# Kernel tuning notes

Measured on AMD Instinct MI355X. Metric: run time of the kernel, lower is better.

## Reference

```python
import jax, jax.numpy as jnp
import numpy as np

N = 4096; D0 = 1024; D1 = 1280; H0 = 819; H1 = 1024; S = 819; K = 5


def setup_inputs() -> dict:
    key = jax.random.key(0)
    ks = jax.random.split(key, 20)
    def rn(k, shape, scale=1.0):
        return jax.random.normal(k, shape, dtype=jnp.float32) * scale
    inp = {}
    inp['x0'] = rn(ks[0], (N, D0))
    inp['x1'] = rn(ks[1], (N, D1))
    inp['we'] = jax.random.uniform(ks[2], (N, 2), dtype=jnp.float32, minval=0.1, maxval=1.0)
    # scale graphs ~1/100 so row-aggregated features stay in tanh's linear-ish range
    inp['g0'] = rn(ks[3], (N, N), 0.01)
    inp['g1'] = rn(ks[4], (N, N), 0.01)
    # Linear weights stored [in, out] (torch Linear applies x @ W.T + b); xavier-ish scale
    inp['We1_0'] = rn(ks[5], (D0, H0), D0 ** -0.5); inp['be1_0'] = jnp.zeros((H0,), jnp.float32)
    inp['We2_0'] = rn(ks[6], (H0, S), H0 ** -0.5);  inp['be2_0'] = jnp.zeros((S,), jnp.float32)
    inp['We1_1'] = rn(ks[7], (D1, H1), D1 ** -0.5); inp['be1_1'] = jnp.zeros((H1,), jnp.float32)
    inp['We2_1'] = rn(ks[8], (H1, S), H1 ** -0.5);  inp['be2_1'] = jnp.zeros((S,), jnp.float32)
    inp['Wd1_0'] = rn(ks[9], (S, H0), S ** -0.5);   inp['bd1_0'] = jnp.zeros((H0,), jnp.float32)
    inp['Wd2_0'] = rn(ks[10], (H0, D0), H0 ** -0.5); inp['bd2_0'] = jnp.zeros((D0,), jnp.float32)
    inp['Wd1_1'] = rn(ks[11], (S, H1), S ** -0.5);  inp['bd1_1'] = jnp.zeros((H1,), jnp.float32)
    inp['Wd2_1'] = rn(ks[12], (H1, D1), H1 ** -0.5); inp['bd2_1'] = jnp.zeros((D1,), jnp.float32)
    inp['Ww_0'] = rn(ks[13], (S, S), S ** -0.5)
    inp['Ww_1'] = rn(ks[14], (S, S), S ** -0.5)
    inp['Wf_0'] = rn(ks[15], (S, S), S ** -0.5)
    inp['Wf_1'] = rn(ks[16], (S, S), S ** -0.5)
    # stands in for the sklearn spectral-clustering centers (constant w.r.t. autodiff)
    inp['cluster_layer'] = rn(ks[17], (K, S), 0.1)
    return inp


def _gconv2(g, x, W1, b1, W2, b2):
    # tanh(Linear(g @ x)) twice: fusable gather-MLP chain
    h1 = jnp.tanh((g @ x) @ W1 + b1)
    return jnp.tanh((g @ h1) @ W2 + b2)


def reference(x0, x1, we, g0, g1,
              We1_0, be1_0, We2_0, be2_0, We1_1, be1_1, We2_1, be2_1,
              Wd1_0, bd1_0, Wd2_0, bd2_0, Wd1_1, bd1_1, Wd2_1, bd2_1,
              Ww_0, Ww_1, Wf_0, Wf_1, cluster_layer):
    # encoders
    h2_0 = _gconv2(g0, x0, We1_0, be1_0, We2_0, be2_0)  # [N, S]
    h2_1 = _gconv2(g1, x1, We1_1, be1_1, We2_1, be2_1)  # [N, S]
    # diag(we[:,i]) @ h_i  ==  broadcast row-scale (avoids O(N^2) diag matmul)
    weighted_sum = we[:, 0:1] * h2_0 + we[:, 1:2] * h2_1
    z = weighted_sum / jnp.sum(we, axis=1, keepdims=True)  # diag(1/sum) @ ws
    # inner-product adjacency decoders
    adj0 = jax.nn.sigmoid((z @ Ww_0) @ z.T)  # [N, N]
    adj1 = jax.nn.sigmoid((z @ Ww_1) @ z.T)
    # feature decoders with fusion weights
    rec0 = _gconv2(g0, jnp.tanh(z @ Wf_0), Wd1_0, bd1_0, Wd2_0, bd2_0)  # [N, D0]
    rec1 = _gconv2(g1, jnp.tanh(z @ Wf_1), Wd1_1, bd1_1, Wd2_1, bd2_1)  # [N, D1]
    # Student-t soft assignment to cluster centers
    d2 = jnp.sum((z[:, None, :] - cluster_layer[None, :, :]) ** 2, axis=2)  # [N, K]
    q = 1.0 / (1.0 + d2)
    q = q / jnp.sum(q, axis=1, keepdims=True)
    # target distribution p
    w = q ** 2 / jnp.sum(q, axis=0)
    p = w / jnp.sum(w, axis=1, keepdims=True)
    return (rec0, rec1, adj0, adj1, z, p, q, cluster_layer)
```

## Files before the change

### kernel.cpp

```cpp
#include <hip/hip_runtime.h>
#include <hip/hip_bf16.h>
#include <cstdint>
#include <cstddef>

typedef __bf16 bf16;
typedef __attribute__((ext_vector_type(8))) __bf16 bf16x8;
typedef __attribute__((ext_vector_type(4))) __bf16 bf16x4;
typedef __attribute__((ext_vector_type(4))) float f32x4;

__device__ __forceinline__ void gload_lds16(const void* g, void* l) {
  __builtin_amdgcn_global_load_lds(
      (const __attribute__((address_space(1))) uint32_t*)(uintptr_t)g,
      (__attribute__((address_space(3))) uint32_t*)(uintptr_t)l, 16, 0, 0);
}

__device__ __forceinline__ float actf(float v, int act) {
  if (act == 1) return tanhf(v);
  if (act == 2) return 1.f / (1.f + __expf(-v));
  return v;
}

struct GProb {
  const bf16* A; const bf16* Bt; const float* bias;
  float* Cf; bf16* Cb; float* Cp;
  int K, Npad, ldcf, ldcb, Ntrue, act;
};
struct GBatch { GProb p[4]; };

template<int SPLIT>
__global__ __launch_bounds__(256, 2)
void gemm_nt_batch(GBatch b)
{
  const int nx = gridDim.x, ny = gridDim.y, nzz = gridDim.z;
  const int total = nx * ny * nzz;
  const int fid = (int)blockIdx.x + nx * ((int)blockIdx.y + ny * (int)blockIdx.z);
  const int q = total >> 3, r = total & 7;
  const int xcd = fid & 7, idx = fid >> 3;
  const int wid = (xcd < r ? xcd * (q + 1) : r * (q + 1) + (xcd - r) * q) + idx;
  const int wx = wid % nx;
  const int rest = wid / nx;
  const int wy = rest % ny;
  const int wz = rest / ny;

  const int prob = (SPLIT == 2) ? (wz >> 1) : wz;
  const int kz   = (SPLIT == 2) ? (wz & 1) : 0;
  const GProb P = b.p[prob];
  const long bn = (long)wx * 128;
  if (bn >= P.Npad) return;

  __shared__ __align__(16) bf16 As[128 * 64];
  __shared__ __align__(16) bf16 Bs[128 * 64];

  const int K    = P.K;
  const int tid  = threadIdx.x;
  const int lane = tid & 63, wave = tid >> 6;
  const int wr = wave >> 1, wc = wave & 1;
  const int l15 = lane & 15, quad = lane >> 4;
  const long bm = (long)wy * 128;

  long aoff[4], boff[4];
  int ldsoff[4];
#pragma unroll
  for (int s = 0; s < 4; ++s) {
    int slot = s * 256 + tid;
    int row = slot >> 3, cs = slot & 7;
    int gc = cs ^ (row & 7);
    aoff[s] = (bm + row) * (long)K + gc * 8;
    boff[s] = (bn + row) * (long)K + gc * 8;
    ldsoff[s] = (s * 256 + wave * 64) * 8;
  }

  const int cfr0 = ((0 * 4 + quad) ^ (l15 & 7)) * 8;
  const int cfr1 = ((1 * 4 + quad) ^ (l15 & 7)) * 8;
  int afr[2][4], bfr[2][4];
#pragma unroll
  for (int i = 0; i < 4; ++i) {
    afr[0][i] = (wr * 64 + i * 16 + l15) * 64 + cfr0;
    afr[1][i] = (wr * 64 + i * 16 + l15) * 64 + cfr1;
    bfr[0][i] = (wc * 64 + i * 16 + l15) * 64 + cfr0;
    bfr[1][i] = (wc * 64 + i * 16 + l15) * 64 + cfr1;
  }

  f32x4 acc[4][4];
#pragma unroll
  for (int i = 0; i < 4; ++i)
#pragma unroll
    for (int j = 0; j < 4; ++j) acc[i][j] = {0.f, 0.f, 0.f, 0.f};

  const int Kseg = K / SPLIT;
  const int kbeg = kz * Kseg;
  for (int k0 = kbeg; k0 < kbeg + Kseg; k0 += 64) {
    __syncthreads();
#pragma unroll
    for (int s = 0; s < 4; ++s) {
      gload_lds16(P.A + aoff[s] + k0, As + ldsoff[s]);
      gload_lds16(P.Bt + boff[s] + k0, Bs + ldsoff[s]);
    }
    __syncthreads();

#pragma unroll
    for (int ks = 0; ks < 2; ++ks) {
      bf16x8 av[4], bv[4];
#pragma unroll
      for (int i = 0; i < 4; ++i) av[i] = *(const bf16x8*)(As + afr[ks][i]);
#pragma unroll
      for (int j = 0; j < 4; ++j) bv[j] = *(const bf16x8*)(Bs + bfr[ks][j]);
#pragma unroll
      for (int i = 0; i < 4; ++i)
#pragma unroll
        for (int j = 0; j < 4; ++j)
          acc[i][j] = __builtin_amdgcn_mfma_f32_16x16x32_bf16(av[i], bv[j], acc[i][j], 0, 0, 0);
    }
  }

  const long row0 = bm + wr * 64 + quad * 4;
  const long col0 = bn + wc * 64 + l15;
  if constexpr (SPLIT == 2) {
    float* Cp = P.Cp + (long)kz * 4096 * P.Npad;
#pragma unroll
    for (int i = 0; i < 4; ++i)
#pragma unroll
      for (int j = 0; j < 4; ++j)
#pragma unroll
        for (int t = 0; t < 4; ++t)
          Cp[(row0 + i * 16 + t) * (long)P.Npad + col0 + j * 16] = acc[i][j][t];
  } else {
    const int act = P.act;
#pragma unroll
    for (int i = 0; i < 4; ++i) {
#pragma unroll
      for (int j = 0; j < 4; ++j) {
        long c = col0 + j * 16;
        float bb = P.bias ? P.bias[c] : 0.f;
#pragma unroll
        for (int t = 0; t < 4; ++t) {
          long r = row0 + i * 16 + t;
          float v = actf(acc[i][j][t] + bb, act);
          if (P.Cf && c < P.Ntrue) P.Cf[r * P.ldcf + c] = v;
          if (P.Cb) P.Cb[r * P.ldcb + c] = (bf16)v;
        }
      }
    }
  }
}

struct CProb {
  const float* part; const float* bias;
  float* Cf; bf16* Cb;
  int Npad, ldcf, ldcb, Ntrue, act;
};
struct CBatch { CProb p[2]; };

__global__ void combine_batch(CBatch cb)
{
  const CProb P = cb.p[blockIdx.z];
  const int row = blockIdx.x;
  const int c4 = threadIdx.x * 4;
  if (c4 >= P.Npad) return;
  const long base = (long)row * P.Npad + c4;
  float4 a = *(const float4*)(P.part + base);
  float4 b = *(const float4*)(P.part + (long)4096 * P.Npad + base);
  float v[4] = {a.x + b.x, a.y + b.y, a.z + b.z, a.w + b.w};
  if (P.bias) {
    float4 bi = *(const float4*)(P.bias + c4);
    v[0] += bi.x; v[1] += bi.y; v[2] += bi.z; v[3] += bi.w;
  }
#pragma unroll
  for (int t = 0; t < 4; ++t) v[t] = actf(v[t], P.act);
  if (P.Cf && c4 < P.Ntrue) {
    float* o = P.Cf + (long)row * P.ldcf + c4;
    o[0] = v[0]; o[1] = v[1]; o[2] = v[2]; o[3] = v[3];
  }
  if (P.Cb) {
    bf16x4 o = {(bf16)v[0], (bf16)v[1], (bf16)v[2], (bf16)v[3]};
    *(bf16x4*)(P.Cb + (long)row * P.ldcb + c4) = o;
  }
}

__global__ void combz(const float* __restrict__ pA, const float* __restrict__ pB,
                      const float* __restrict__ bA, const float* __restrict__ bB,
                      const float* __restrict__ we, float* __restrict__ zout,
                      bf16* __restrict__ zb)
{
  const int n = blockIdx.x;
  const int c = threadIdx.x * 4;
  const long base = (long)n * 896 + c;
  const long half = (long)4096 * 896;
  float4 a0 = *(const float4*)(pA + base);
  float4 a1 = *(const float4*)(pA + half + base);
  float4 b0 = *(const float4*)(pB + base);
  float4 b1 = *(const float4*)(pB + half + base);
  float4 ba = *(const float4*)(bA + c);
  float4 bb = *(const float4*)(bB + c);
  const float w0 = we[n * 2], w1 = we[n * 2 + 1];
  const float inv = 1.f / (w0 + w1);
  float h0[4] = {a0.x + a1.x + ba.x, a0.y + a1.y + ba.y, a0.z + a1.z + ba.z, a0.w + a1.w + ba.w};
  float h1[4] = {b0.x + b1.x + bb.x, b0.y + b1.y + bb.y, b0.z + b1.z + bb.z, b0.w + b1.w + bb.w};
  bf16x4 o;
#pragma unroll
  for (int t = 0; t < 4; ++t) {
    float v = (w0 * tanhf(h0[t]) + w1 * tanhf(h1[t])) * inv;
    o[t] = (bf16)v;
    if (c + t < 819) zout[(long)n * 819 + c + t] = v;
  }
  *(bf16x4*)(zb + base) = o;
}

struct TrBatch {
  const void* src[14]; bf16* dst[14];
  int R[14], C[14], Q[14], nbx[14], isb[14];
  int blkStart[15];
  int nprob;
};

__global__ void tr_batch(TrBatch a)
{
  __shared__ float tile[32][33];
  int pi = 0, b = blockIdx.x;
  while (b >= a.blkStart[pi + 1]) ++pi;
  const int rel = b - a.blkStart[pi];
  const int nbx = a.nbx[pi];
  const int q0 = (rel % nbx) * 32;
  const int p0 = (rel / nbx) * 32;
  const int R = a.R[pi], C = a.C[pi], Q = a.Q[pi];
  const bool isb = a.isb[pi] != 0;
  const void* src = a.src[pi];
  const int tx = threadIdx.x & 31, ty = threadIdx.x >> 5;
#pragma unroll
  for (int y = ty; y < 32; y += 8) {
    int r = q0 + y, c = p0 + tx;
    float v = 0.f;
    if (r < R && c < C)
      v = isb ? (float)((const bf16*)src)[(long)r * C + c]
              : ((const float*)src)[(long)r * C + c];
    tile[y][tx] = v;
  }
  __syncthreads();
  bf16* dst = a.dst[pi];
#pragma unroll
  for (int y = ty; y < 32; y += 8)
    dst[(long)(p0 + y) * Q + (q0 + tx)] = (bf16)tile[tx][y];
}

struct CvtB { const float* s[4]; bf16* d[4]; long n[4]; };
__global__ void cvt_batch(CvtB cb)
{
  const float* s = cb.s[blockIdx.z];
  bf16* d = cb.d[blockIdx.z];
  long i = ((long)blockIdx.x * blockDim.x + threadIdx.x) * 4;
  if (i >= cb.n[blockIdx.z]) return;
  float4 v = *(const float4*)(s + i);
  bf16x4 o = {(bf16)v.x, (bf16)v.y, (bf16)v.z, (bf16)v.w};
  *(bf16x4*)(d + i) = o;
}

__global__ void qkern(const float* __restrict__ z, const float* __restrict__ cl,
                      float* __restrict__ qout)
{
  const int n = blockIdx.x;
  const int lane = threadIdx.x;
  float d0 = 0, d1 = 0, d2 = 0, d3 = 0, d4 = 0;
  for (int s = lane; s < 819; s += 64) {
    float zv = z[(long)n * 819 + s];
    float t0 = zv - cl[0 * 819 + s]; d0 += t0 * t0;
    float t1 = zv - cl[1 * 819 + s]; d1 += t1 * t1;
    float t2 = zv - cl[2 * 819 + s]; d2 += t2 * t2;
    float t3 = zv - cl[3 * 819 + s]; d3 += t3 * t3;
    float t4 = zv - cl[4 * 819 + s]; d4 += t4 * t4;
  }
#pragma unroll
  for (int off = 32; off > 0; off >>= 1) {
    d0 += __shfl_xor(d0, off);
    d1 += __shfl_xor(d1, off);
    d2 += __shfl_xor(d2, off);
    d3 += __shfl_xor(d3, off);
    d4 += __shfl_xor(d4, off);
  }
  if (lane == 0) {
    float q0 = 1.f / (1.f + d0), q1 = 1.f / (1.f + d1), q2 = 1.f / (1.f + d2);
    float q3 = 1.f / (1.f + d3), q4 = 1.f / (1.f + d4);
    float inv = 1.f / (q0 + q1 + q2 + q3 + q4);
    float* qr = qout + (long)n * 5;
    qr[0] = q0 * inv; qr[1] = q1 * inv; qr[2] = q2 * inv;
    qr[3] = q3 * inv; qr[4] = q4 * inv;
  }
}

__global__ void colsum_kern(const float* __restrict__ q, float* __restrict__ colsum)
{
  __shared__ float red[256];
  const int k = blockIdx.x;
  float s = 0.f;
  for (int n = threadIdx.x; n < 4096; n += 256) s += q[(long)n * 5 + k];
  red[threadIdx.x] = s;
  __syncthreads();
  for (int w = 128; w > 0; w >>= 1) {
    if (threadIdx.x < w) red[threadIdx.x] += red[threadIdx.x + w];
    __syncthreads();
  }
  if (threadIdx.x == 0) colsum[k] = red[0];
}

__global__ void pkern(const float* __restrict__ q, const float* __restrict__ colsum,
                      float* __restrict__ p)
{
  int n = blockIdx.x * blockDim.x + threadIdx.x;
  if (n >= 4096) return;
  float w[5], s = 0.f;
#pragma unroll
  for (int k = 0; k < 5; ++k) {
    float qv = q[(long)n * 5 + k];
    w[k] = qv * qv / colsum[k];
    s += w[k];
  }
  float inv = 1.f / s;
#pragma unroll
  for (int k = 0; k < 5; ++k) p[(long)n * 5 + k] = w[k] * inv;
}

struct BiasArgs {
  const float* src[8];
  float* dst[8];
  int n[8];
  int np[8];
};

__global__ void biaspad(BiasArgs a)
{
  int b = blockIdx.x;
  for (int i = threadIdx.x; i < a.np[b]; i += blockDim.x)
    a.dst[b][i] = (i < a.n[b]) ? a.src[b][i] : 0.f;
}

extern "C" void kernel_launch(void* const* d_in, const int* in_sizes, int n_in,
                              void* d_out, int out_size, void* d_ws, size_t ws_size,
                              hipStream_t stream)
{
  (void)in_sizes; (void)n_in; (void)out_size; (void)ws_size;
  const float* x0    = (const float*)d_in[0];
  const float* x1    = (const float*)d_in[1];
  const float* we    = (const float*)d_in[2];
  const float* g0    = (const float*)d_in[3];
  const float* g1    = (const float*)d_in[4];
  const float* We1_0 = (const float*)d_in[5];
  const float* be1_0 = (const float*)d_in[6];
  const float* We2_0 = (const float*)d_in[7];
  const float* be2_0 = (const float*)d_in[8];
  const float* We1_1 = (const float*)d_in[9];
  const float* be1_1 = (const float*)d_in[10];
  const float* We2_1 = (const float*)d_in[11];
  const float* be2_1 = (const float*)d_in[12];
  const float* Wd1_0 = (const float*)d_in[13];
  const float* bd1_0 = (const float*)d_in[14];
  const float* Wd2_0 = (const float*)d_in[15];
  const float* bd2_0 = (const float*)d_in[16];
  const float* Wd1_1 = (const float*)d_in[17];
  const float* bd1_1 = (const float*)d_in[18];
  const float* Wd2_1 = (const float*)d_in[19];
  const float* bd2_1 = (const float*)d_in[20];
  const float* Ww0   = (const float*)d_in[21];
  const float* Ww1   = (const float*)d_in[22];
  const float* Wf0   = (const float*)d_in[23];
  const float* Wf1   = (const float*)d_in[24];
  const float* clus  = (const float*)d_in[25];
  float* out = (float*)d_out;

  const size_t OFF_REC0 = 0;
  const size_t OFF_REC1 = 4194304;
  const size_t OFF_ADJ0 = 9437184;
  const size_t OFF_ADJ1 = 26214400;
  const size_t OFF_Z    = 42991616;
  const size_t OFF_P    = 46346240;
  const size_t OFF_Q    = 46366720;
  const size_t OFF_CL   = 46387200;

  char* ws = (char*)d_ws;
  size_t off = 0;
  auto alloc = [&](size_t bytes) -> void* {
    off = (off + 255) & ~(size_t)255;
    void* p = ws + off;
    off += bytes;
    return p;
  };
  const long N = 4096;
  bf16* g0b   = (bf16*)alloc((size_t)N * 4096 * 2);
  bf16* g1b   = (bf16*)alloc((size_t)N * 4096 * 2);
  bf16* x0b   = (bf16*)alloc((size_t)N * 1024 * 2);
  bf16* x1b   = (bf16*)alloc((size_t)N * 1280 * 2);
  bf16* BTe10 = (bf16*)alloc((size_t)896 * 1024 * 2);
  bf16* BTe20 = (bf16*)alloc((size_t)896 * 896 * 2);
  bf16* BTe11 = (bf16*)alloc((size_t)1024 * 1280 * 2);
  bf16* BTe21 = (bf16*)alloc((size_t)896 * 1024 * 2);
  bf16* BTd10 = (bf16*)alloc((size_t)896 * 896 * 2);
  bf16* BTd20 = (bf16*)alloc((size_t)1024 * 896 * 2);
  bf16* BTd11 = (bf16*)alloc((size_t)1024 * 896 * 2);
  bf16* BTd21 = (bf16*)alloc((size_t)1280 * 1024 * 2);
  bf16* BTw0  = (bf16*)alloc((size_t)896 * 896 * 2);
  bf16* BTw1  = (bf16*)alloc((size_t)896 * 896 * 2);
  bf16* BTf0  = (bf16*)alloc((size_t)896 * 896 * 2);
  bf16* BTf1  = (bf16*)alloc((size_t)896 * 896 * 2);
  float* pbe10 = (float*)alloc(896 * 4);
  float* pbe20 = (float*)alloc(896 * 4);
  float* pbe11 = (float*)alloc(1024 * 4);
  float* pbe21 = (float*)alloc(896 * 4);
  float* pbd10 = (float*)alloc(896 * 4);
  float* pbd20 = (float*)alloc(1024 * 4);
  float* pbd11 = (float*)alloc(1024 * 4);
  float* pbd21 = (float*)alloc(1280 * 4);
  bf16* zb     = (bf16*)alloc((size_t)N * 896 * 2);
  float* colsum = (float*)alloc(64);
  bf16* xT0 = (bf16*)alloc((size_t)1024 * 4096 * 2);
  bf16* xT1 = (bf16*)alloc((size_t)1280 * 4096 * 2);
  bf16* u0  = (bf16*)alloc((size_t)N * 1024 * 2);
  bf16* u1  = (bf16*)alloc((size_t)N * 1280 * 2);
  bf16* h0  = (bf16*)alloc((size_t)N * 896 * 2);
  bf16* h1b = (bf16*)alloc((size_t)N * 1024 * 2);
  bf16* y0  = (bf16*)alloc((size_t)N * 896 * 2);
  bf16* y1  = (bf16*)alloc((size_t)N * 896 * 2);
  bf16* t0b = (bf16*)alloc((size_t)N * 896 * 2);
  bf16* t1b = (bf16*)alloc((size_t)N * 896 * 2);
  float* partA = (float*)alloc((size_t)2 * N * 1024 * 4);
  float* partB = (float*)alloc((size_t)2 * N * 1024 * 4);

  {
    CvtB cb;
    cb.s[0] = g0; cb.d[0] = g0b; cb.n[0] = N * 4096;
    cb.s[1] = g1; cb.d[1] = g1b; cb.n[1] = N * 4096;
    cb.s[2] = x0; cb.d[2] = x0b; cb.n[2] = N * 1024;
    cb.s[3] = x1; cb.d[3] = x1b; cb.n[3] = N * 1280;
    cvt_batch<<<dim3(16384, 1, 4), 256, 0, stream>>>(cb);
  }

  {
    TrBatch tb{};
    tb.nprob = 0; tb.blkStart[0] = 0;
    auto addTr = [&](const void* s, bf16* d, int R, int C, int P, int Q, int isb) {
      int i = tb.nprob++;
      tb.src[i] = s; tb.dst[i] = d;
      tb.R[i] = R; tb.C[i] = C; tb.Q[i] = Q; tb.isb[i] = isb;
      tb.nbx[i] = Q / 32;
      tb.blkStart[i + 1] = tb.blkStart[i] + (Q / 32) * (P / 32);
    };
    addTr(We1_0, BTe10, 1024, 819, 896, 1024, 0);
    addTr(We2_0, BTe20, 819, 819, 896, 896, 0);
    addTr(We1_1, BTe11, 1280, 1024, 1024, 1280, 0);
    addTr(We2_1, BTe21, 1024, 819, 896, 1024, 0);
    addTr(Wd1_0, BTd10, 819, 819, 896, 896, 0);
    addTr(Wd2_0, BTd20, 819, 1024, 1024, 896, 0);
    addTr(Wd1_1, BTd11, 819, 1024, 1024, 896, 0);
    addTr(Wd2_1, BTd21, 1024, 1280, 1280, 1024, 0);
    addTr(Ww0, BTw0, 819, 819, 896, 896, 0);
    addTr(Ww1, BTw1, 819, 819, 896, 896, 0);
    addTr(Wf0, BTf0, 819, 819, 896, 896, 0);
    addTr(Wf1, BTf1, 819, 819, 896, 896, 0);
    tr_batch<<<tb.blkStart[tb.nprob], 256, 0, stream>>>(tb);
  }

  BiasArgs ba;
  {
    const float* bsrc[8] = {be1_0, be2_0, be1_1, be2_1, bd1_0, bd2_0, bd1_1, bd2_1};
    float* bdst[8] = {pbe10, pbe20, pbe11, pbe21, pbd10, pbd20, pbd11, pbd21};
    int bn_[8] = {819, 819, 1024, 819, 819, 1024, 1024, 1280};
    int bnp[8] = {896, 896, 1024, 896, 896, 1024, 1024, 1280};
    for (int i = 0; i < 8; ++i) { ba.src[i] = bsrc[i]; ba.dst[i] = bdst[i]; ba.n[i] = bn_[i]; ba.np[i] = bnp[i]; }
  }
  biaspad<<<8, 256, 0, stream>>>(ba);

  GBatch gb{};
  int np = 0, maxN = 0;
  auto beg = [&]() { np = 0; maxN = 0; gb = GBatch{}; };
  auto add = [&](const bf16* A, const bf16* Bt, const float* bias,
                 float* Cf, int ldcf, bf16* Cb, int ldcb,
                 int K, int Npad, int Ntrue, int act) {
    gb.p[np].A = A; gb.p[np].Bt = Bt; gb.p[np].bias = bias;
    gb.p[np].Cf = Cf; gb.p[np].Cb = Cb; gb.p[np].Cp = nullptr;
    gb.p[np].K = K; gb.p[np].Npad = Npad;
    gb.p[np].ldcf = ldcf; gb.p[np].ldcb = ldcb;
    gb.p[np].Ntrue = Ntrue; gb.p[np].act = act;
    ++np;
    if (Npad > maxN) maxN = Npad;
  };
  auto addS = [&](const bf16* A, const bf16* Bt, float* Cp, int K, int Npad) {
    gb.p[np].A = A; gb.p[np].Bt = Bt; gb.p[np].bias = nullptr;
    gb.p[np].Cf = nullptr; gb.p[np].Cb = nullptr; gb.p[np].Cp = Cp;
    gb.p[np].K = K; gb.p[np].Npad = Npad;
    gb.p[np].ldcf = 0; gb.p[np].ldcb = 0; gb.p[np].Ntrue = 0; gb.p[np].act = 0;
    ++np;
    if (Npad > maxN) maxN = Npad;
  };
  auto goN = [&]() { gemm_nt_batch<1><<<dim3(maxN / 128, 32, np), 256, 0, stream>>>(gb); };
  auto goS = [&]() { gemm_nt_batch<2><<<dim3(maxN / 128, 32, np * 2), 256, 0, stream>>>(gb); };
  auto comb = [&](const float* bias0, float* Cf0, int ldf0, int Nt0, bf16* Cb0, int ldb0, int Np0, int act0,
                  const float* bias1, float* Cf1, int ldf1, int Nt1, bf16* Cb1, int ldb1, int Np1, int act1) {
    CBatch cb;
    cb.p[0] = {partA, bias0, Cf0, Cb0, Np0, ldf0, ldb0, Nt0, act0};
    cb.p[1] = {partB, bias1, Cf1, Cb1, Np1, ldf1, ldb1, Nt1, act1};
    combine_batch<<<dim3(4096, 1, 2), 256, 0, stream>>>(cb);
  };
  auto trb2 = [&](const bf16* s0, int C0, const bf16* s1, int C1) {
    TrBatch tb{};
    tb.nprob = 2; tb.blkStart[0] = 0;
    tb.src[0] = s0; tb.dst[0] = xT0; tb.R[0] = 4096; tb.C[0] = C0; tb.Q[0] = 4096;
    tb.isb[0] = 1; tb.nbx[0] = 128; tb.blkStart[1] = 128 * (C0 / 32);
    tb.src[1] = s1; tb.dst[1] = xT1; tb.R[1] = 4096; tb.C[1] = C1; tb.Q[1] = 4096;
    tb.isb[1] = 1; tb.nbx[1] = 128; tb.blkStart[2] = tb.blkStart[1] + 128 * (C1 / 32);
    tr_batch<<<tb.blkStart[2], 256, 0, stream>>>(tb);
  };

  beg();
  add(x0b, BTe10, nullptr, nullptr, 0, u0, 896, 1024, 896, 896, 0);
  add(x1b, BTe11, nullptr, nullptr, 0, u1, 1024, 1280, 1024, 1024, 0);
  goN();
  trb2(u0, 896, u1, 1024);
  beg();
  addS(g0b, xT0, partA, 4096, 896);
  addS(g1b, xT1, partB, 4096, 1024);
  goS();
  comb(pbe10, nullptr, 0, 0, h0, 896, 896, 1,
       pbe11, nullptr, 0, 0, h1b, 1024, 1024, 1);
  beg();
  add(h0, BTe20, nullptr, nullptr, 0, u0, 896, 896, 896, 896, 0);
  add(h1b, BTe21, nullptr, nullptr, 0, u1, 896, 1024, 896, 896, 0);
  goN();
  trb2(u0, 896, u1, 896);
  beg();
  addS(g0b, xT0, partA, 4096, 896);
  addS(g1b, xT1, partB, 4096, 896);
  goS();
  combz<<<4096, 224, 0, stream>>>(partA, partB, pbe20, pbe21, we, out + OFF_Z, zb);

  beg();
  add(zb, BTw0, nullptr, nullptr, 0, y0, 896, 896, 896, 896, 0);
  add(zb, BTw1, nullptr, nullptr, 0, y1, 896, 896, 896, 896, 0);
  add(zb, BTf0, nullptr, nullptr, 0, t0b, 896, 896, 896, 896, 1);
  add(zb, BTf1, nullptr, nullptr, 0, t1b, 896, 896, 896, 896, 1);
  goN();
  beg();
  add(y0, zb, nullptr, out + OFF_ADJ0, 4096, nullptr, 0, 896, 4096, 4096, 2);
  add(y1, zb, nullptr, out + OFF_ADJ1, 4096, nullptr, 0, 896, 4096, 4096, 2);
  goN();

  trb2(t0b, 896, t1b, 896);
  beg();
  addS(g0b, xT0, partA, 4096, 896);
  addS(g1b, xT1, partB, 4096, 896);
  goS();
  comb(nullptr, nullptr, 0, 0, u0, 896, 896, 0,
       nullptr, nullptr, 0, 0, u1, 896, 896, 0);
  beg();
  add(u0, BTd10, pbd10, nullptr, 0, h0, 896, 896, 896, 896, 1);
  add(u1, BTd11, pbd11, nullptr, 0, h1b, 1024, 896, 1024, 1024, 1);
  goN();
  trb2(h0, 896, h1b, 1024);
  beg();
  addS(g0b, xT0, partA, 4096, 896);
  addS(g1b, xT1, partB, 4096, 1024);
  goS();
  comb(nullptr, nullptr, 0, 0, u0, 896, 896, 0,
       nullptr, nullptr, 0, 0, u1, 1024, 1024, 0);
  beg();
  add(u0, BTd20, pbd20, out + OFF_REC0, 1024, nullptr, 0, 896, 1024, 1024, 1);
  add(u1, BTd21, pbd21, out + OFF_REC1, 1280, nullptr, 0, 1024, 1280, 1280, 1);
  goN();

  qkern<<<4096, 64, 0, stream>>>(out + OFF_Z, clus, out + OFF_Q);
  colsum_kern<<<5, 256, 0, stream>>>(out + OFF_Q, colsum);
  pkern<<<16, 256, 0, stream>>>(out + OFF_Q, colsum, out + OFF_P);
  hipMemcpyAsync(out + OFF_CL, (const void*)clus, 4095 * sizeof(float),
                 hipMemcpyDeviceToDevice, stream);
}
```

Before: 1.072 ms.

## Emit transposed GEMM outputs directly and flatten batched GEMM grid scheduling

The small feature-transform GEMMs are computed as W^T·X^T so they write the transposed operand for the graph aggregation directly. This removes the four separate transpose kernels and the intermediate buffers they used, and adds a row-bias mode so bias is still applied in the transposed layout. The batched GEMM also moves from a padded 3D grid (maxN x 32 x np) to a flat 1D grid with per-problem start offsets, so no early-exit blocks are launched when problem sizes differ. In exchange, each block pays for a small problem-lookup loop and the transposed-output writes may have different coalescing.

After: 1.057 ms. Within noise of the previous version (-1.4%).

```diff
diff --git a/kernel.cpp b/kernel.cpp
--- a/kernel.cpp
+++ b/kernel.cpp
@@ -23,40 +23,34 @@
 struct GProb {
   const bf16* A; const bf16* Bt; const float* bias;
   float* Cf; bf16* Cb; float* Cp;
-  int K, Npad, ldcf, ldcb, Ntrue, act;
+  int lda, kbeg, kcnt, nbx, ldcf, ldcb, Ntrue, act, biasRow;
 };
-struct GBatch { GProb p[4]; };
-
-template<int SPLIT>
+struct GBatch { GProb p[4]; int start[5]; };
+
 __global__ __launch_bounds__(256, 2)
 void gemm_nt_batch(GBatch b)
 {
-  const int nx = gridDim.x, ny = gridDim.y, nzz = gridDim.z;
-  const int total = nx * ny * nzz;
-  const int fid = (int)blockIdx.x + nx * ((int)blockIdx.y + ny * (int)blockIdx.z);
-  const int q = total >> 3, r = total & 7;
+  const int T = (int)gridDim.x;
+  const int fid = (int)blockIdx.x;
+  const int q = T >> 3, r = T & 7;
   const int xcd = fid & 7, idx = fid >> 3;
   const int wid = (xcd < r ? xcd * (q + 1) : r * (q + 1) + (xcd - r) * q) + idx;
-  const int wx = wid % nx;
-  const int rest = wid / nx;
-  const int wy = rest % ny;
-  const int wz = rest / ny;
-
-  const int prob = (SPLIT == 2) ? (wz >> 1) : wz;
-  const int kz   = (SPLIT == 2) ? (wz & 1) : 0;
-  const GProb P = b.p[prob];
-  const long bn = (long)wx * 128;
-  if (bn >= P.Npad) return;
+
+  int pi = 0;
+  while (wid >= b.start[pi + 1]) ++pi;
+  const GProb P = b.p[pi];
+  const int rel = wid - b.start[pi];
+  const long bn = (long)(rel % P.nbx) * 128;
+  const long bm = (long)(rel / P.nbx) * 128;
 
   __shared__ __align__(16) bf16 As[128 * 64];
   __shared__ __align__(16) bf16 Bs[128 * 64];
 
-  const int K    = P.K;
+  const int lda  = P.lda;
   const int tid  = threadIdx.x;
   const int lane = tid & 63, wave = tid >> 6;
   const int wr = wave >> 1, wc = wave & 1;
   const int l15 = lane & 15, quad = lane >> 4;
-  const long bm = (long)wy * 128;
 
   long aoff[4], boff[4];
   int ldsoff[4];
@@ -65,8 +59,8 @@
     int slot = s * 256 + tid;
     int row = slot >> 3, cs = slot & 7;
     int gc = cs ^ (row & 7);
-    aoff[s] = (bm + row) * (long)K + gc * 8;
-    boff[s] = (bn + row) * (long)K + gc * 8;
+    aoff[s] = (bm + row) * (long)lda + gc * 8;
+    boff[s] = (bn + row) * (long)lda + gc * 8;
     ldsoff[s] = (s * 256 + wave * 64) * 8;
   }
 
@@ -87,9 +81,7 @@
 #pragma unroll
     for (int j = 0; j < 4; ++j) acc[i][j] = {0.f, 0.f, 0.f, 0.f};
 
-  const int Kseg = K / SPLIT;
-  const int kbeg = kz * Kseg;
-  for (int k0 = kbeg; k0 < kbeg + Kseg; k0 += 64) {
+  for (int k0 = P.kbeg; k0 < P.kbeg + P.kcnt; k0 += 64) {
     __syncthreads();
 #pragma unroll
     for (int s = 0; s < 4; ++s) {
@@ -115,15 +107,15 @@
 
   const long row0 = bm + wr * 64 + quad * 4;
   const long col0 = bn + wc * 64 + l15;
-  if constexpr (SPLIT == 2) {
-    float* Cp = P.Cp + (long)kz * 4096 * P.Npad;
+  if (P.Cp) {
+    const int ldp = P.nbx * 128;
 #pragma unroll
     for (int i = 0; i < 4; ++i)
 #pragma unroll
       for (int j = 0; j < 4; ++j)
 #pragma unroll
         for (int t = 0; t < 4; ++t)
-          Cp[(row0 + i * 16 + t) * (long)P.Npad + col0 + j * 16] = acc[i][j][t];
+          P.Cp[(row0 + i * 16 + t) * (long)ldp + col0 + j * 16] = acc[i][j][t];
   } else {
     const int act = P.act;
 #pragma unroll
@@ -131,10 +123,11 @@
 #pragma unroll
       for (int j = 0; j < 4; ++j) {
         long c = col0 + j * 16;
-        float bb = P.bias ? P.bias[c] : 0.f;
+        float bbc = (P.bias && !P.biasRow) ? P.bias[c] : 0.f;
 #pragma unroll
         for (int t = 0; t < 4; ++t) {
           long r = row0 + i * 16 + t;
+          float bb = P.biasRow ? (P.bias ? P.bias[r] : 0.f) : bbc;
           float v = actf(acc[i][j][t] + bb, act);
           if (P.Cf && c < P.Ntrue) P.Cf[r * P.ldcf + c] = v;
           if (P.Cb) P.Cb[r * P.ldcb + c] = (bf16)v;
@@ -417,8 +410,6 @@
   bf16* h1b = (bf16*)alloc((size_t)N * 1024 * 2);
   bf16* y0  = (bf16*)alloc((size_t)N * 896 * 2);
   bf16* y1  = (bf16*)alloc((size_t)N * 896 * 2);
-  bf16* t0b = (bf16*)alloc((size_t)N * 896 * 2);
-  bf16* t1b = (bf16*)alloc((size_t)N * 896 * 2);
   float* partA = (float*)alloc((size_t)2 * N * 1024 * 4);
   float* partB = (float*)alloc((size_t)2 * N * 1024 * 4);
 
@@ -467,29 +458,36 @@
   biaspad<<<8, 256, 0, stream>>>(ba);
 
   GBatch gb{};
-  int np = 0, maxN = 0;
-  auto beg = [&]() { np = 0; maxN = 0; gb = GBatch{}; };
+  int np = 0, tot = 0;
+  auto beg = [&]() { np = 0; tot = 0; gb = GBatch{}; gb.start[0] = 0; };
+  auto addE = [&](const bf16* A, const bf16* Bt, const float* bias, int biasRow,
+                  float* Cf, int ldcf, int Ntrue, bf16* Cb, int ldcb,
+                  float* Cp, int lda, int kbeg, int kcnt, int M, int Nn, int act) {
+    GProb& p = gb.p[np];
+    p.A = A; p.Bt = Bt; p.bias = bias; p.Cf = Cf; p.Cb = Cb; p.Cp = Cp;
+    p.lda = lda; p.kbeg = kbeg; p.kcnt = kcnt; p.nbx = Nn / 128;
+    p.ldcf = ldcf; p.ldcb = ldcb; p.Ntrue = Ntrue; p.act = act; p.biasRow = biasRow;
+    tot += (Nn / 128) * (M / 128);
+    ++np; gb.start[np] = tot;
+  };
   auto add = [&](const bf16* A, const bf16* Bt, const float* bias,
-                 float* Cf, int ldcf, bf16* Cb, int ldcb,
-                 int K, int Npad, int Ntrue, int act) {
-    gb.p[np].A = A; gb.p[np].Bt = Bt; gb.p[np].bias = bias;
-    gb.p[np].Cf = Cf; gb.p[np].Cb = Cb; gb.p[np].Cp = nullptr;
-    gb.p[np].K = K; gb.p[np].Npad = Npad;
-    gb.p[np].ldcf = ldcf; gb.p[np].ldcb = ldcb;
-    gb.p[np].Ntrue = Ntrue; gb.p[np].act = act;
-    ++np;
-    if (Npad > maxN) maxN = Npad;
-  };
-  auto addS = [&](const bf16* A, const bf16* Bt, float* Cp, int K, int Npad) {
-    gb.p[np].A = A; gb.p[np].Bt = Bt; gb.p[np].bias = nullptr;
-    gb.p[np].Cf = nullptr; gb.p[np].Cb = nullptr; gb.p[np].Cp = Cp;
-    gb.p[np].K = K; gb.p[np].Npad = Npad;
-    gb.p[np].ldcf = 0; gb.p[np].ldcb = 0; gb.p[np].Ntrue = 0; gb.p[np].act = 0;
-    ++np;
-    if (Npad > maxN) maxN = Npad;
-  };
-  auto goN = [&]() { gemm_nt_batch<1><<<dim3(maxN / 128, 32, np), 256, 0, stream>>>(gb); };
-  auto goS = [&]() { gemm_nt_batch<2><<<dim3(maxN / 128, 32, np * 2), 256, 0, stream>>>(gb); };
+                 float* Cf, int ldcf, int Ntrue, bf16* Cb, int ldcb,
+                 int K, int M, int Nn, int act) {
+    addE(A, Bt, bias, 0, Cf, ldcf, Ntrue, Cb, ldcb, nullptr, K, 0, K, M, Nn, act);
+  };
+  auto addT = [&](const bf16* A, const bf16* Bt, const float* biasR,
+                  bf16* Ct, int K, int M, int act) {
+    addE(A, Bt, biasR, 1, nullptr, 0, 0, Ct, 4096, nullptr, K, 0, K, M, 4096, act);
+  };
+  auto addS = [&](const bf16* A, const bf16* Bt, float* Cp, int K, int Nn) {
+    addE(A, Bt, nullptr, 0, nullptr, 0, 0, nullptr, 0, Cp, K, 0, K / 2, 4096, Nn, 0);
+    addE(A, Bt, nullptr, 0, nullptr, 0, 0, nullptr, 0,
+         Cp + (size_t)4096 * Nn, K, K / 2, K / 2, 4096, Nn, 0);
+  };
+  auto go = [&]() {
+    for (int k = np; k < 4; ++k) gb.start[k + 1] = tot;
+    gemm_nt_batch<<<tot, 256, 0, stream>>>(gb);
+  };
   auto comb = [&](const float* bias0, float* Cf0, int ldf0, int Nt0, bf16* Cb0, int ldb0, int Np0, int act0,
                   const float* bias1, float* Cf1, int ldf1, int Nt1, bf16* Cb1, int ldb1, int Np1, int act1) {
     CBatch cb;
@@ -497,71 +495,58 @@
     cb.p[1] = {partB, bias1, Cf1, Cb1, Np1, ldf1, ldb1, Nt1, act1};
     combine_batch<<<dim3(4096, 1, 2), 256, 0, stream>>>(cb);
   };
-  auto trb2 = [&](const bf16* s0, int C0, const bf16* s1, int C1) {
-    TrBatch tb{};
-    tb.nprob = 2; tb.blkStart[0] = 0;
-    tb.src[0] = s0; tb.dst[0] = xT0; tb.R[0] = 4096; tb.C[0] = C0; tb.Q[0] = 4096;
-    tb.isb[0] = 1; tb.nbx[0] = 128; tb.blkStart[1] = 128 * (C0 / 32);
-    tb.src[1] = s1; tb.dst[1] = xT1; tb.R[1] = 4096; tb.C[1] = C1; tb.Q[1] = 4096;
-    tb.isb[1] = 1; tb.nbx[1] = 128; tb.blkStart[2] = tb.blkStart[1] + 128 * (C1 / 32);
-    tr_batch<<<tb.blkStart[2], 256, 0, stream>>>(tb);
-  };
-
-  beg();
-  add(x0b, BTe10, nullptr, nullptr, 0, u0, 896, 1024, 896, 896, 0);
-  add(x1b, BTe11, nullptr, nullptr, 0, u1, 1024, 1280, 1024, 1024, 0);
-  goN();
-  trb2(u0, 896, u1, 1024);
+
+  beg();
+  addT(BTe10, x0b, nullptr, xT0, 1024, 896, 0);
+  addT(BTe11, x1b, nullptr, xT1, 1280, 1024, 0);
+  go();
   beg();
   addS(g0b, xT0, partA, 4096, 896);
   addS(g1b, xT1, partB, 4096, 1024);
-  goS();
+  go();
   comb(pbe10, nullptr, 0, 0, h0, 896, 896, 1,
        pbe11, nullptr, 0, 0, h1b, 1024, 1024, 1);
   beg();
-  add(h0, BTe20, nullptr, nullptr, 0, u0, 896, 896, 896, 896, 0);
-  add(h1b, BTe21, nullptr, nullptr, 0, u1, 896, 1024, 896, 896, 0);
-  goN();
-  trb2(u0, 896, u1, 896);
+  addT(BTe20, h0, nullptr, xT0, 896, 896, 0);
+  addT(BTe21, h1b, nullptr, xT1, 1024, 896, 0);
+  go();
   beg();
   addS(g0b, xT0, partA, 4096, 896);
   addS(g1b, xT1, partB, 4096, 896);
-  goS();
+  go();
   combz<<<4096, 224, 0, stream>>>(partA, partB, pbe20, pbe21, we, out + OFF_Z, zb);
 
   beg();
-  add(zb, BTw0, nullptr, nullptr, 0, y0, 896, 896, 896, 896, 0);
-  add(zb, BTw1, nullptr, nullptr, 0, y1, 896, 896, 896, 896, 0);
-  add(zb, BTf0, nullptr, nullptr, 0, t0b, 896, 896, 896, 896, 1);
-  add(zb, BTf1, nullptr, nullptr, 0, t1b, 896, 896, 896, 896, 1);
-  goN();
-  beg();
-  add(y0, zb, nullptr, out + OFF_ADJ0, 4096, nullptr, 0, 896, 4096, 4096, 2);
-  add(y1, zb, nullptr, out + OFF_ADJ1, 4096, nullptr, 0, 896, 4096, 4096, 2);
-  goN();
-
-  trb2(t0b, 896, t1b, 896);
+  add(zb, BTw0, nullptr, nullptr, 0, 0, y0, 896, 896, 4096, 896, 0);
+  add(zb, BTw1, nullptr, nullptr, 0, 0, y1, 896, 896, 4096, 896, 0);
+  addT(BTf0, zb, nullptr, xT0, 896, 896, 1);
+  addT(BTf1, zb, nullptr, xT1, 896, 896, 1);
+  go();
+  beg();
+  add(y0, zb, nullptr, out + OFF_ADJ0, 4096, 4096, nullptr, 0, 896, 4096, 4096, 2);
+  add(y1, zb, nullptr, out + OFF_ADJ1, 4096, 4096, nullptr, 0, 896, 4096, 4096, 2);
+  go();
+
   beg();
   addS(g0b, xT0, partA, 4096, 896);
   addS(g1b, xT1, partB, 4096, 896);
-  goS();
+  go();
   comb(nullptr, nullptr, 0, 0, u0, 896, 896, 0,
        nullptr, nullptr, 0, 0, u1, 896, 896, 0);
   beg();
-  add(u0, BTd10, pbd10, nullptr, 0, h0, 896, 896, 896, 896, 1);
-  add(u1, BTd11, pbd11, nullptr, 0, h1b, 1024, 896, 1024, 1024, 1);
-  goN();
-  trb2(h0, 896, h1b, 1024);
+  addT(BTd10, u0, pbd10, xT0, 896, 896, 1);
+  addT(BTd11, u1, pbd11, xT1, 896, 1024, 1);
+  go();
   beg();
   addS(g0b, xT0, partA, 4096, 896);
   addS(g1b, xT1, partB, 4096, 1024);
-  goS();
+  go();
   comb(nullptr, nullptr, 0, 0, u0, 896, 896, 0,
        nullptr, nullptr, 0, 0, u1, 1024, 1024, 0);
   beg();
-  add(u0, BTd20, pbd20, out + OFF_REC0, 1024, nullptr, 0, 896, 1024, 1024, 1);
-  add(u1, BTd21, pbd21, out + OFF_REC1, 1280, nullptr, 0, 1024, 1280, 1280, 1);
-  goN();
+  add(u0, BTd20, pbd20, out + OFF_REC0, 1024, 1024, nullptr, 0, 896, 4096, 1024, 1);
+  add(u1, BTd21, pbd21, out + OFF_REC1, 1280, 1280, nullptr, 0, 1024, 4096, 1280, 1);
+  go();
 
   qkern<<<4096, 64, 0, stream>>>(out + OFF_Z, clus, out + OFF_Q);
   colsum_kern<<<5, 256, 0, stream>>>(out + OFF_Q, colsum);
```
